# Optimization experiments

Measured on AMD Instinct MI355X. Metric: run time of the kernel, lower is better.

## Reference

```python
import jax, jax.numpy as jnp
import numpy as np

B, S, T, H, VS, VT = 64, 64, 64, 1024, 32000, 32000


def _init(key, shape, scale=0.05):
    return scale * jax.random.normal(key, shape, dtype=jnp.float32)


def setup_inputs() -> dict:
    key = jax.random.key(0)
    ks = jax.random.split(key, 16)
    source = jax.random.randint(ks[0], (B, S), 0, VS)
    target = jax.random.randint(ks[1], (B, T), 0, VT)
    emb_src = _init(ks[2], (VS, H)).at[0].set(0.0)   # padding_idx=0
    emb_tgt = _init(ks[3], (VT, H)).at[0].set(0.0)   # padding_idx=0
    W_ih_enc = _init(ks[4], (4 * H, H)); W_hh_enc = _init(ks[5], (4 * H, H))
    b_ih_enc = _init(ks[6], (4 * H,));   b_hh_enc = _init(ks[7], (4 * H,))
    W_ih_dec = _init(ks[8], (4 * H, H)); W_hh_dec = _init(ks[9], (4 * H, H))
    b_ih_dec = _init(ks[10], (4 * H,));  b_hh_dec = _init(ks[11], (4 * H,))
    W_att = _init(ks[12], (H, 2 * H));   b_att = _init(ks[13], (H,))
    W_out = _init(ks[14], (VT, H));      b_out = _init(ks[15], (VT,))
    return dict(source=source, target=target, emb_src=emb_src, emb_tgt=emb_tgt,
                W_ih_enc=W_ih_enc, W_hh_enc=W_hh_enc, b_ih_enc=b_ih_enc, b_hh_enc=b_hh_enc,
                W_ih_dec=W_ih_dec, W_hh_dec=W_hh_dec, b_ih_dec=b_ih_dec, b_hh_dec=b_hh_dec,
                W_att=W_att, b_att=b_att, W_out=W_out, b_out=b_out)


def _lstm_cell(x, h, c, W_ih, W_hh, b):
    # PyTorch gate order: i, f, g, o
    gates = x @ W_ih.T + h @ W_hh.T + b
    i, f, g, o = jnp.split(gates, 4, axis=-1)
    c_new = jax.nn.sigmoid(f) * c + jax.nn.sigmoid(i) * jnp.tanh(g)
    h_new = jax.nn.sigmoid(o) * jnp.tanh(c_new)
    return h_new, c_new


def reference(source, target, emb_src, emb_tgt,
              W_ih_enc, W_hh_enc, b_ih_enc, b_hh_enc,
              W_ih_dec, W_hh_dec, b_ih_dec, b_hh_dec,
              W_att, b_att, W_out, b_out):
    src = source.T              # [S, B]
    tgt = target.T              # [T, B]
    h0 = jnp.zeros((B, H), jnp.float32)
    c0 = jnp.zeros((B, H), jnp.float32)

    # ---- Encoder: time-major LSTM via scan (dropout in eval mode = identity) ----
    x_src = emb_src[src]        # [S, B, H]
    b_enc = b_ih_enc + b_hh_enc

    def enc_step(carry, x_t):
        h, c = carry
        h, c = _lstm_cell(x_t, h, c, W_ih_enc, W_hh_enc, b_enc)
        return (h, c), h

    (hT, cT), hx_list = jax.lax.scan(enc_step, (h0, c0), x_src)  # hx_list: [S, B, H]

    # ---- Decoder: hx_cx is never updated in the original loop, so every
    # timestep uses the SAME encoder final state -> fully vectorizable over t ----
    words_f = tgt[: S - 1]      # [Td, B], Td = T-1 (S == T)
    words_t = tgt[1:]           # [Td, B]
    x_dec = emb_tgt[words_f]    # [Td, B, H]
    b_dec = b_ih_dec + b_hh_dec
    gates = x_dec @ W_ih_dec.T + (hT @ W_hh_dec.T + b_dec)[None]  # [Td, B, 4H]
    i, f, g, o = jnp.split(gates, 4, axis=-1)
    c_new = jax.nn.sigmoid(f) * cT[None] + jax.nn.sigmoid(i) * jnp.tanh(g)
    hx = jax.nn.sigmoid(o) * jnp.tanh(c_new)                       # [Td, B, H]

    # ---- Attention (dot-product over source positions, softmax over S) ----
    scores = jnp.einsum('tbh,sbh->tsb', hx, hx_list)               # [Td, S, B]
    neg_inf = jnp.asarray(-jnp.inf, jnp.float32)
    mask = (src != 0)[None]                                        # [1, S, B]
    scores = jnp.where(mask, scores, neg_inf)
    align = jax.nn.softmax(scores, axis=1)                         # over S
    content = jnp.einsum('tsb,sbh->tbh', align, hx_list)           # [Td, B, H]
    concat = jnp.concatenate([content, hx], axis=-1)               # [Td, B, 2H]
    hx_att = jnp.tanh(concat @ W_att.T + b_att)                    # [Td, B, H]

    # ---- Output projection + per-step cross entropy (ignore_index=0), summed ----
    logits = hx_att @ W_out.T + b_out                              # [Td, B, VT]
    logp = jax.nn.log_softmax(logits, axis=-1)
    nll = -jnp.take_along_axis(logp, words_t[..., None], axis=-1).squeeze(-1)  # [Td, B]
    valid = (words_t != 0).astype(jnp.float32)
    per_step = jnp.sum(nll * valid, axis=1) / jnp.maximum(jnp.sum(valid, axis=1), 1.0)
    return jnp.sum(per_step)
```

## Files before the change

### kernel.cpp

```cpp
#include <hip/hip_runtime.h>
#include <math.h>

#define Bb 64
#define Ss 64
#define Hh 1024
#define Vv 32000
#define RD 4032
#define RP 4096
#define NT4 4096
#define ENC_NBLK 64

typedef unsigned short u16;
typedef unsigned long long u64;
typedef __attribute__((ext_vector_type(8))) short bf16x8;
typedef __attribute__((ext_vector_type(4))) float f32x4;

#define MFMA(a, b, c) __builtin_amdgcn_mfma_f32_16x16x32_bf16(a, b, c, 0, 0, 0)

__device__ __forceinline__ u16 f2b(float f) {
  union { float f; unsigned u; } v; v.f = f;
  unsigned r = v.u + 0x7fffu + ((v.u >> 16) & 1u);
  return (u16)(r >> 16);
}
__device__ __forceinline__ float b2f(u16 b) {
  union { unsigned u; float f; } v; v.u = ((unsigned)b) << 16; return v.f;
}
__device__ __forceinline__ float sigf(float x) { return 1.f / (1.f + expf(-x)); }

__device__ __forceinline__ u64 AL(const u64* p) {
  return __hip_atomic_load(p, __ATOMIC_RELAXED, __HIP_MEMORY_SCOPE_AGENT);
}
__device__ __forceinline__ void AS(u64* p, u64 v) {
  __hip_atomic_store(p, v, __ATOMIC_RELAXED, __HIP_MEMORY_SCOPE_AGENT);
}
__device__ __forceinline__ int AL32(const int* p) {
  return __hip_atomic_load(p, __ATOMIC_RELAXED, __HIP_MEMORY_SCOPE_AGENT);
}
__device__ __forceinline__ void AS32(int* p, int v) {
  __hip_atomic_store(p, v, __ATOMIC_RELAXED, __HIP_MEMORY_SCOPE_AGENT);
}

__device__ __forceinline__ void gll16(const void* g, void* l) {
  __builtin_amdgcn_global_load_lds(
      (const __attribute__((address_space(1))) unsigned int*)g,
      (__attribute__((address_space(3))) unsigned int*)l, 16, 0, 0);
}

__global__ void k_fail(float* out) { out[0] = 1e30f; }

__global__ void k_cvt(const float* __restrict__ in, u16* __restrict__ out, int n4) {
  int i = blockIdx.x * blockDim.x + threadIdx.x;
  const int st = gridDim.x * blockDim.x;
  for (; i < n4; i += st) {
    float4 v = ((const float4*)in)[i];
    ushort4 o; o.x = f2b(v.x); o.y = f2b(v.y); o.z = f2b(v.z); o.w = f2b(v.w);
    ((ushort4*)out)[i] = o;
  }
}

__global__ void k_gather(const int* __restrict__ tok, const float* __restrict__ emb,
                         u16* __restrict__ outp, int nstep) {
  const int r = blockIdx.x;
  const int step = r >> 6, b = r & 63;
  const int idx = (step < nstep) ? tok[b * 64 + step] : 0;
  const float4 v = ((const float4*)(emb + (size_t)idx * Hh))[threadIdx.x];
  ushort4 o; o.x = f2b(v.x); o.y = f2b(v.y); o.z = f2b(v.z); o.w = f2b(v.w);
  ((ushort4*)(outp + (size_t)r * Hh))[threadIdx.x] = o;
}

__device__ __forceinline__ void dg_tile(const u16* __restrict__ A, const u16* __restrict__ Bm,
                                        u16* __restrict__ C, int bx, int by,
                                        u16* As, u16* Bs) {
  const int tid = threadIdx.x;
  const int wave = tid >> 6, lane = tid & 63;
  const int l15 = lane & 15, lhi = lane >> 4;
  const int m0 = by * 128, n0 = bx * 128;
  const int wm = (wave >> 1) * 64, wn = (wave & 1) * 64;
  f32x4 acc[4][4] = {};
  const int srow = wave * 32 + (lane >> 3);
  const int scolb = (lane & 7) * 16;
  for (int k0 = 0; k0 < Hh; k0 += 64) {
    __syncthreads();
#pragma unroll
    for (int q = 0; q < 4; ++q) {
      const int r = srow + q * 8;
      gll16((const char*)(A + (size_t)(m0 + r) * Hh + k0) + scolb,
            (char*)As + (wave * 32 + q * 8) * 128);
      gll16((const char*)(Bm + (size_t)(n0 + r) * Hh + k0) + scolb,
            (char*)Bs + (wave * 32 + q * 8) * 128);
    }
    __syncthreads();
#pragma unroll
    for (int kk = 0; kk < 2; ++kk) {
      const int ko = kk * 32 + lhi * 8;
      bf16x8 af[4], bfr[4];
#pragma unroll
      for (int i = 0; i < 4; ++i) af[i] = *(const bf16x8*)(As + (wm + i * 16 + l15) * 64 + ko);
#pragma unroll
      for (int j = 0; j < 4; ++j) bfr[j] = *(const bf16x8*)(Bs + (wn + j * 16 + l15) * 64 + ko);
#pragma unroll
      for (int i = 0; i < 4; ++i)
#pragma unroll
        for (int j = 0; j < 4; ++j)
          acc[i][j] = MFMA(af[i], bfr[j], acc[i][j]);
    }
  }
#pragma unroll
  for (int i = 0; i < 4; ++i) {
    const int gr = m0 + wm + i * 16 + lhi * 4;
#pragma unroll
    for (int j = 0; j < 4; ++j) {
      const int gc = n0 + wn + j * 16 + l15;
#pragma unroll
      for (int rr = 0; rr < 4; ++rr)
        C[(size_t)(gr + rr) * NT4 + gc] = f2b(acc[i][j][rr]);
    }
  }
}

__global__ __launch_bounds__(256)
void k_pre(const u16* __restrict__ A, const u16* __restrict__ Bm, u16* __restrict__ C) {
  __shared__ __align__(16) u16 As[128 * 64];
  __shared__ __align__(16) u16 Bs[128 * 64];
  const int t = blockIdx.x;
  dg_tile(A, Bm, C, t & 31, t >> 5, As, Bs);
}

template<int EPI>
__global__ __launch_bounds__(256)
void k_gemm(const u16* __restrict__ A, const u16* __restrict__ Bm,
            void* __restrict__ C, int M, int N, int K,
            const float* __restrict__ bias,
            float* __restrict__ pmax, float* __restrict__ psum, int ncols) {
  __shared__ __align__(16) u16 As[128 * 64];
  __shared__ __align__(16) u16 Bs[128 * 64];
  const int tid = threadIdx.x;
  const int wave = tid >> 6, lane = tid & 63;
  const int l15 = lane & 15, lhi = lane >> 4;
  int bx = blockIdx.x, by = blockIdx.y;
  {
    const int gx_ = gridDim.x, gy_ = gridDim.y;
    const int nwg = gx_ * gy_;
    if ((gy_ & 3) == 0 && (gx_ & 1) == 0) {
      const int f = by * gx_ + bx;
      const int x = f & 7, i = f >> 3;
      const int rby = gy_ >> 2, hx = gx_ >> 1;
      by = (x >> 1) * rby + (i % rby);
      bx = (x & 1) * hx + (i / rby);
    } else if ((nwg & 7) == 0) {
      int flat = by * gx_ + bx;
      const int qq = nwg >> 3;
      flat = (flat & 7) * qq + (flat >> 3);
      bx = flat % gx_; by = flat / gx_;
    }
  }
  const int m0 = by * 128, n0 = bx * 128;
  const int wm = (wave >> 1) * 64, wn = (wave & 1) * 64;
  f32x4 acc[4][4] = {};
  const int srow = wave * 32 + (lane >> 3);
  const int scolb = (lane & 7) * 16;

  for (int k0 = 0; k0 < K; k0 += 64) {
    __syncthreads();
#pragma unroll
    for (int q = 0; q < 4; ++q) {
      const int r = srow + q * 8;
      int ra = m0 + r; ra = (ra < M) ? ra : (M - 1);
      gll16((const char*)(A + (size_t)ra * K + k0) + scolb,
            (char*)As + (wave * 32 + q * 8) * 128);
      gll16((const char*)(Bm + (size_t)(n0 + r) * K + k0) + scolb,
            (char*)Bs + (wave * 32 + q * 8) * 128);
    }
    __syncthreads();
#pragma unroll
    for (int kk = 0; kk < 2; ++kk) {
      const int ko = kk * 32 + lhi * 8;
      bf16x8 af[4], bfr[4];
#pragma unroll
      for (int i = 0; i < 4; ++i) af[i] = *(const bf16x8*)(As + (wm + i * 16 + l15) * 64 + ko);
#pragma unroll
      for (int j = 0; j < 4; ++j) bfr[j] = *(const bf16x8*)(Bs + (wn + j * 16 + l15) * 64 + ko);
#pragma unroll
      for (int i = 0; i < 4; ++i)
#pragma unroll
        for (int j = 0; j < 4; ++j)
          acc[i][j] = MFMA(af[i], bfr[j], acc[i][j]);
    }
  }

  if (EPI == 0) {
#pragma unroll
    for (int i = 0; i < 4; ++i) {
      const int gr = m0 + wm + i * 16 + lhi * 4;
#pragma unroll
      for (int j = 0; j < 4; ++j) {
        const int gc = n0 + wn + j * 16 + l15;
        const float bv = bias ? bias[gc] : 0.f;
#pragma unroll
        for (int rr = 0; rr < 4; ++rr)
          ((float*)C)[(size_t)(gr + rr) * N + gc] = acc[i][j][rr] + bv;
      }
    }
  } else if (EPI == 3) {
#pragma unroll
    for (int i = 0; i < 4; ++i) {
      const int gr = m0 + wm + i * 16 + lhi * 4;
#pragma unroll
      for (int j = 0; j < 4; ++j) {
        const int gc = n0 + wn + j * 16 + l15;
        const float bv = bias[gc];
#pragma unroll
        for (int rr = 0; rr < 4; ++rr)
          ((u16*)C)[(size_t)(gr + rr) * N + gc] = f2b(tanhf(acc[i][j][rr] + bv));
      }
    }
  } else {
    float bj[4];
#pragma unroll
    for (int j = 0; j < 4; ++j) bj[j] = bias[n0 + wn + j * 16 + l15];
    const int pc = bx * 2 + (wn ? 1 : 0);
#pragma unroll
    for (int i = 0; i < 4; ++i) {
#pragma unroll
      for (int rr = 0; rr < 4; ++rr) {
        float v0 = acc[i][0][rr] + bj[0];
        float v1 = acc[i][1][rr] + bj[1];
        float v2 = acc[i][2][rr] + bj[2];
        float v3 = acc[i][3][rr] + bj[3];
        float m = fmaxf(fmaxf(v0, v1), fmaxf(v2, v3));
#pragma unroll
        for (int d = 1; d < 16; d <<= 1) m = fmaxf(m, __shfl_xor(m, d, 64));
        float s = __expf(v0 - m) + __expf(v1 - m) + __expf(v2 - m) + __expf(v3 - m);
#pragma unroll
        for (int d = 1; d < 16; d <<= 1) s += __shfl_xor(s, d, 64);
        if (l15 == 0) {
          const int grow = m0 + wm + i * 16 + lhi * 4 + rr;
          pmax[(size_t)grow * ncols + pc] = m;
          psum[(size_t)grow * ncols + pc] = s;
        }
      }
    }
  }
}

__global__ __launch_bounds__(256, 1)
void k_enc_all(const u16* __restrict__ Wb, const u16* __restrict__ gx,
               const float* __restrict__ b_ih, const float* __restrict__ b_hh,
               u16* __restrict__ hxl, float* __restrict__ c_out, int* flags) {
  __shared__ __align__(16) u16 Ws[64 * 1024];
  __shared__ float Gs[64 * 65];
  __shared__ float bsum[64];
  const int tid = threadIdx.x;
  const int wave = tid >> 6, lane = tid & 63;
  const int l15 = lane & 15, lhi = lane >> 4;
  const int c0 = blockIdx.x * 16;
  const int cb = tid >> 2, cq = tid & 3;
  const int rot = blockIdx.x & 31;

  for (int i = tid; i < 64 * 128; i += 256) {
    const int r = i >> 7, ck = i & 127;
    const int grow = (r >> 4) * Hh + c0 + (r & 15);
    const int bo = (ck * 16) ^ ((r & 7) << 4);
    *(bf16x8*)((char*)Ws + r * 2048 + bo) = *(const bf16x8*)(Wb + (size_t)grow * Hh + ck * 8);
  }
  if (tid < 64) {
    const int col = (tid >> 4) * Hh + c0 + (tid & 15);
    bsum[tid] = b_ih[col] + b_hh[col];
  }
  float creg[4] = {0.f, 0.f, 0.f, 0.f};
  __syncthreads();

  for (int s = 0; s < 64; ++s) {
    u64 graw[4];
#pragma unroll
    for (int g = 0; g < 4; ++g)
      graw[g] = *(const u64*)(gx + (size_t)(s * 64 + cb) * NT4 + g * Hh + c0 + cq * 4);

    f32x4 acc[4] = {};
    if (s > 0) {
      if (wave == 0) {
        for (;;) {
          const int f = AL32(flags + blockIdx.x * 64 + lane);
          if (__all(f >= s)) break;
          __builtin_amdgcn_s_sleep(1);
        }
      }
      __syncthreads();
      const u64* apw = (const u64*)(hxl + ((size_t)(s - 1) * 64 + wave * 16 + l15) * Hh);
      const char* wsb = (const char*)Ws;
      const int xr = (l15 & 7) << 4;
#pragma unroll 8
      for (int i = 0; i < 32; ++i) {
        const int kf = (i + rot) & 31;
        const int k = kf * 32 + lhi * 8;
        const u64 ua = AL(apw + (k >> 2));
        const u64 ub = AL(apw + (k >> 2) + 1);
        union { u64 qq[2]; bf16x8 v; } cv;
        cv.qq[0] = ua; cv.qq[1] = ub;
        const int kb = (k * 2) ^ xr;
#pragma unroll
        for (int nt = 0; nt < 4; ++nt)
          acc[nt] = MFMA(cv.v, *(const bf16x8*)(wsb + (nt * 16 + l15) * 2048 + kb), acc[nt]);
      }
    }
#pragma unroll
    for (int nt = 0; nt < 4; ++nt)
#pragma unroll
      for (int r = 0; r < 4; ++r)
        Gs[(wave * 16 + lhi * 4 + r) * 65 + nt * 16 + l15] = acc[nt][r];
    __syncthreads();
    {
      const float* gsrow = Gs + cb * 65;
      u64 pk = 0;
#pragma unroll
      for (int j = 0; j < 4; ++j) {
        const int col = cq * 4 + j;
        const float gi = gsrow[col]      + b2f((u16)(graw[0] >> (16 * j))) + bsum[col];
        const float gf = gsrow[16 + col] + b2f((u16)(graw[1] >> (16 * j))) + bsum[16 + col];
        const float gg = gsrow[32 + col] + b2f((u16)(graw[2] >> (16 * j))) + bsum[32 + col];
        const float go = gsrow[48 + col] + b2f((u16)(graw[3] >> (16 * j))) + bsum[48 + col];
        const float cn = sigf(gf) * creg[j] + sigf(gi) * tanhf(gg);
        const float hv = sigf(go) * tanhf(cn);
        creg[j] = cn;
        pk |= (u64)f2b(hv) << (16 * j);
      }
      AS((u64*)(hxl + ((size_t)s * 64 + cb) * Hh + c0 + cq * 4), pk);
    }
    __syncthreads();
    if (tid < ENC_NBLK)
      AS32(flags + tid * 64 + blockIdx.x, s + 1);
  }
#pragma unroll
  for (int j = 0; j < 4; ++j)
    c_out[cb * Hh + c0 + cq * 4 + j] = creg[j];
}

__global__ void k_dec_cell(const u16* __restrict__ G, const float* __restrict__ dbase,
                           const float* __restrict__ cT, const float* __restrict__ b_ih,
                           const float* __restrict__ b_hh, u16* __restrict__ Acat) {
  const int idx = blockIdx.x * 256 + threadIdx.x;
  const int r = idx >> 8, c4 = (idx & 255) * 4;
  if (r >= RD) return;
  const int b = r & 63;
  u64 graw[4]; f32x4 dv[4], bi[4], bh[4];
#pragma unroll
  for (int g = 0; g < 4; ++g) {
    graw[g] = *(const u64*)(G + (size_t)r * NT4 + g * Hh + c4);
    dv[g] = *(const f32x4*)(dbase + (size_t)b * NT4 + g * Hh + c4);
    bi[g] = *(const f32x4*)(b_ih + g * Hh + c4);
    bh[g] = *(const f32x4*)(b_hh + g * Hh + c4);
  }
  const f32x4 cv4 = *(const f32x4*)(cT + b * Hh + c4);
  u64 pk = 0;
#pragma unroll
  for (int j = 0; j < 4; ++j) {
    const float gi = b2f((u16)(graw[0] >> (16 * j))) + dv[0][j] + bi[0][j] + bh[0][j];
    const float gf = b2f((u16)(graw[1] >> (16 * j))) + dv[1][j] + bi[1][j] + bh[1][j];
    const float gg = b2f((u16)(graw[2] >> (16 * j))) + dv[2][j] + bi[2][j] + bh[2][j];
    const float go = b2f((u16)(graw[3] >> (16 * j))) + dv[3][j] + bi[3][j] + bh[3][j];
    const float cn = sigf(gf) * cv4[j] + sigf(gi) * tanhf(gg);
    const float hv = sigf(go) * tanhf(cn);
    pk |= (u64)f2b(hv) << (16 * j);
  }
  *(u64*)(Acat + (size_t)r * 2048 + Hh + c4) = pk;
}

__global__ __launch_bounds__(256)
void k_attn(u16* Acat, const u16* __restrict__ hxl, const int* __restrict__ src) {
  __shared__ float qs[Hh];
  __shared__ float sc[Ss];
  const int r = blockIdx.x;
  const int b = r & 63;
  const int tid = threadIdx.x, wave = tid >> 6, lane = tid & 63;
  for (int h = tid; h < Hh; h += 256) qs[h] = b2f(Acat[(size_t)r * 2048 + Hh + h]);
  __syncthreads();
  for (int sub = 0; sub < 16; ++sub) {
    const int ss = wave * 16 + sub;
    const ushort4* hp4 = (const ushort4*)(hxl + ((size_t)ss * Bb + b) * Hh);
    float p = 0.f;
#pragma unroll
    for (int q = 0; q < 4; ++q) {
      const int i4 = lane + 64 * q;
      const ushort4 v = hp4[i4];
      p += qs[i4 * 4 + 0] * b2f(v.x) + qs[i4 * 4 + 1] * b2f(v.y)
         + qs[i4 * 4 + 2] * b2f(v.z) + qs[i4 * 4 + 3] * b2f(v.w);
    }
#pragma unroll
    for (int d = 1; d < 64; d <<= 1) p += __shfl_xor(p, d, 64);
    if (lane == 0) sc[ss] = (src[b * 64 + ss] != 0) ? p : -INFINITY;
  }
  __syncthreads();
  if (wave == 0) {
    const float v = sc[lane];
    float m = v;
#pragma unroll
    for (int d = 1; d < 64; d <<= 1) m = fmaxf(m, __shfl_xor(m, d, 64));
    const float e = __expf(v - m);
    float ssum = e;
#pragma unroll
    for (int d = 1; d < 64; d <<= 1) ssum += __shfl_xor(ssum, d, 64);
    sc[lane] = e / ssum;
  }
  __syncthreads();
  float4 a4 = {0.f, 0.f, 0.f, 0.f};
  for (int s2 = 0; s2 < 64; ++s2) {
    const float a = sc[s2];
    const ushort4 v = *(const ushort4*)(hxl + ((size_t)s2 * Bb + b) * Hh + tid * 4);
    a4.x += a * b2f(v.x); a4.y += a * b2f(v.y);
    a4.z += a * b2f(v.z); a4.w += a * b2f(v.w);
  }
  u16* dst = Acat + (size_t)r * 2048 + tid * 4;
  dst[0] = f2b(a4.x); dst[1] = f2b(a4.y); dst[2] = f2b(a4.z); dst[3] = f2b(a4.w);
}

__global__ void k_lsetl(const float* __restrict__ pmax, const float* __restrict__ psum,
                        const u16* __restrict__ hx_att_b, const int* __restrict__ target,
                        const float* __restrict__ W, const float* __restrict__ bo,
                        float* __restrict__ nll, int ncols) {
  const int r = blockIdx.x * 4 + (threadIdx.x >> 6);
  const int lane = threadIdx.x & 63;
  if (r >= RD) return;
  float m = -INFINITY;
  for (int i = lane; i < ncols; i += 64) m = fmaxf(m, pmax[(size_t)r * ncols + i]);
#pragma unroll
  for (int d = 1; d < 64; d <<= 1) m = fmaxf(m, __shfl_xor(m, d, 64));
  float s = 0.f;
  for (int i = lane; i < ncols; i += 64)
    s += psum[(size_t)r * ncols + i] * __expf(pmax[(size_t)r * ncols + i] - m);
#pragma unroll
  for (int d = 1; d < 64; d <<= 1) s += __shfl_xor(s, d, 64);
  const int t = r >> 6, b = r & 63;
  const int w = target[b * 64 + t + 1];
  const u16* a = hx_att_b + (size_t)r * Hh;
  const float* wr = W + (size_t)w * Hh;
  float p = 0.f;
  for (int h = lane; h < Hh; h += 64) p += b2f(a[h]) * wr[h];
#pragma unroll
  for (int d = 1; d < 64; d <<= 1) p += __shfl_xor(p, d, 64);
  if (lane == 0) nll[r] = (m + logf(s)) - (p + bo[w]);
}

__global__ void k_final(const float* __restrict__ nll, const int* __restrict__ target,
                        float* __restrict__ out) {
  const int t = threadIdx.x;
  float ps = 0.f;
  if (t < 63) {
    float sn = 0.f, cnt = 0.f;
    for (int b = 0; b < 64; ++b) {
      const int r = t * 64 + b;
      const int w = target[b * 64 + t + 1];
      if (w != 0) { sn += nll[r]; cnt += 1.f; }
    }
    ps = sn / fmaxf(cnt, 1.f);
  }
#pragma unroll
  for (int d = 1; d < 64; d <<= 1) ps += __shfl_xor(ps, d, 64);
  if (t == 0) out[0] = ps;
}

extern "C" void kernel_launch(void* const* d_in, const int* in_sizes, int n_in,
                              void* d_out, int out_size, void* d_ws, size_t ws_size,
                              hipStream_t stream) {
  const int*   source   = (const int*)d_in[0];
  const int*   target   = (const int*)d_in[1];
  const float* emb_src  = (const float*)d_in[2];
  const float* emb_tgt  = (const float*)d_in[3];
  const float* W_ih_enc = (const float*)d_in[4];
  const float* W_hh_enc = (const float*)d_in[5];
  const float* b_ih_enc = (const float*)d_in[6];
  const float* b_hh_enc = (const float*)d_in[7];
  const float* W_ih_dec = (const float*)d_in[8];
  const float* W_hh_dec = (const float*)d_in[9];
  const float* b_ih_dec = (const float*)d_in[10];
  const float* b_hh_dec = (const float*)d_in[11];
  const float* W_att    = (const float*)d_in[12];
  const float* b_att    = (const float*)d_in[13];
  const float* W_out    = (const float*)d_in[14];
  const float* b_out    = (const float*)d_in[15];
  float* out = (float*)d_out;

  char* base = (char*)d_ws;
  size_t off = 0;
  auto alloc = [&](size_t bytes) -> void* {
    void* r = base + off; off += (bytes + 255) & ~(size_t)255; return r;
  };
  u16*   wb_ih_enc = (u16*)alloc((size_t)NT4 * Hh * 2);
  u16*   wb_hh_enc = (u16*)alloc((size_t)NT4 * Hh * 2);
  u16*   wb_ih_dec = (u16*)alloc((size_t)NT4 * Hh * 2);
  u16*   wb_hh_dec = (u16*)alloc((size_t)NT4 * Hh * 2);
  u16*   wb_att    = (u16*)alloc((size_t)Hh * 2048 * 2);
  u16*   wb_out    = (u16*)alloc((size_t)Vv * Hh * 2);
  u16*   x_src_b   = (u16*)alloc((size_t)RP * Hh * 2);
  u16*   x_dec_b   = (u16*)alloc((size_t)RP * Hh * 2);
  u16*   gates16   = (u16*)alloc((size_t)RP * NT4 * 2);
  u16*   gates_dec = (u16*)alloc((size_t)RP * NT4 * 2);
  u16*   hxl       = (u16*)alloc((size_t)Ss * Bb * Hh * 2);
  float* c_enc     = (float*)alloc((size_t)Bb * Hh * 4);
  float* dbase     = (float*)alloc((size_t)128 * NT4 * 4);
  u16*   Acat      = (u16*)alloc((size_t)RP * 2048 * 2);
  u16*   hx_att_b  = (u16*)alloc((size_t)RP * Hh * 2);
  float* pmax      = (float*)alloc((size_t)RP * 500 * 4);
  float* psum      = (float*)alloc((size_t)RP * 500 * 4);
  float* nll       = (float*)alloc((size_t)RD * 4);
  int*   flags     = (int*)alloc(ENC_NBLK * ENC_NBLK * 4);

  if (off > ws_size) { k_fail<<<1, 1, 0, stream>>>(out); return; }

  k_cvt<<<2048, 256, 0, stream>>>(W_ih_enc, wb_ih_enc, NT4 * Hh / 4);
  k_cvt<<<2048, 256, 0, stream>>>(W_hh_enc, wb_hh_enc, NT4 * Hh / 4);
  k_cvt<<<2048, 256, 0, stream>>>(W_ih_dec, wb_ih_dec, NT4 * Hh / 4);
  k_cvt<<<2048, 256, 0, stream>>>(W_hh_dec, wb_hh_dec, NT4 * Hh / 4);
  k_cvt<<<2048, 256, 0, stream>>>(W_att, wb_att, Hh * 2048 / 4);
  k_cvt<<<2048, 256, 0, stream>>>(W_out, wb_out, Vv * Hh / 4);

  hipMemsetAsync(flags, 0, ENC_NBLK * ENC_NBLK * 4, stream);

  k_gather<<<RP, 256, 0, stream>>>(source, emb_src, x_src_b, 64);
  k_gather<<<RP, 256, 0, stream>>>(target, emb_tgt, x_dec_b, 63);

  k_pre<<<1024, 256, 0, stream>>>(x_src_b, wb_ih_enc, gates16);
  k_enc_all<<<ENC_NBLK, 256, 0, stream>>>(wb_hh_enc, gates16, b_ih_enc, b_hh_enc,
                                          hxl, c_enc, flags);

  k_pre<<<1024, 256, 0, stream>>>(x_dec_b, wb_ih_dec, gates_dec);
  k_gemm<0><<<dim3(32, 1), 256, 0, stream>>>(hxl + (size_t)63 * Bb * Hh, wb_hh_dec, dbase,
                                             64, NT4, Hh, nullptr, nullptr, nullptr, 0);
  k_dec_cell<<<RD, 256, 0, stream>>>(gates_dec, dbase, c_enc, b_ih_dec, b_hh_dec, Acat);

  k_attn<<<RD, 256, 0, stream>>>(Acat, hxl, source);

  k_gemm<3><<<dim3(8, 32), 256, 0, stream>>>(Acat, wb_att, hx_att_b, RP, Hh, 2048,
                                             b_att, nullptr, nullptr, 0);

  k_gemm<2><<<dim3(250, 32), 256, 0, stream>>>(hx_att_b, wb_out, nullptr, RP, Vv, Hh,
                                               b_out, pmax, psum, 500);
  k_lsetl<<<(RD + 3) / 4, 256, 0, stream>>>(pmax, psum, hx_att_b, target, W_out, b_out,
                                            nll, 500);
  k_final<<<1, 64, 0, stream>>>(nll, target, out);
}
```

Before: 1.522 ms.

## Merge prep launches and stage encoder states in LDS for attention

```diff
diff --git a/kernel.cpp b/kernel.cpp
--- a/kernel.cpp
+++ b/kernel.cpp
@@ -48,19 +48,39 @@
 
 __global__ void k_fail(float* out) { out[0] = 1e30f; }
 
-__global__ void k_cvt(const float* __restrict__ in, u16* __restrict__ out, int n4) {
-  int i = blockIdx.x * blockDim.x + threadIdx.x;
+__global__ void k_cvt_all(const float* __restrict__ s0, u16* __restrict__ d0,
+                          const float* __restrict__ s1, u16* __restrict__ d1,
+                          const float* __restrict__ s2, u16* __restrict__ d2,
+                          const float* __restrict__ s3, u16* __restrict__ d3,
+                          const float* __restrict__ s4, u16* __restrict__ d4,
+                          const float* __restrict__ s5, u16* __restrict__ d5) {
+  const int A4 = NT4 * Hh / 4;
+  const int E4 = Hh * 2048 / 4;
+  const int F4 = Vv * Hh / 4;
+  const int TOT = 4 * A4 + E4 + F4;
   const int st = gridDim.x * blockDim.x;
-  for (; i < n4; i += st) {
-    float4 v = ((const float4*)in)[i];
+  for (int i = blockIdx.x * blockDim.x + threadIdx.x; i < TOT; i += st) {
+    const float* sp; u16* dp; int off;
+    if (i < A4)            { sp = s0; dp = d0; off = i; }
+    else if (i < 2 * A4)   { sp = s1; dp = d1; off = i - A4; }
+    else if (i < 3 * A4)   { sp = s2; dp = d2; off = i - 2 * A4; }
+    else if (i < 4 * A4)   { sp = s3; dp = d3; off = i - 3 * A4; }
+    else if (i < 4 * A4 + E4) { sp = s4; dp = d4; off = i - 4 * A4; }
+    else                   { sp = s5; dp = d5; off = i - 4 * A4 - E4; }
+    const float4 v = ((const float4*)sp)[off];
     ushort4 o; o.x = f2b(v.x); o.y = f2b(v.y); o.z = f2b(v.z); o.w = f2b(v.w);
-    ((ushort4*)out)[i] = o;
-  }
-}
-
-__global__ void k_gather(const int* __restrict__ tok, const float* __restrict__ emb,
-                         u16* __restrict__ outp, int nstep) {
-  const int r = blockIdx.x;
+    ((ushort4*)dp)[off] = o;
+  }
+}
+
+__global__ void k_gather2(const int* __restrict__ src_tok, const float* __restrict__ emb_s,
+                          u16* __restrict__ out_s,
+                          const int* __restrict__ tgt_tok, const float* __restrict__ emb_t,
+                          u16* __restrict__ out_t) {
+  int r = blockIdx.x;
+  const int* tok; const float* emb; u16* outp; int nstep;
+  if (r < RP) { tok = src_tok; emb = emb_s; outp = out_s; nstep = 64; }
+  else        { r -= RP; tok = tgt_tok; emb = emb_t; outp = out_t; nstep = 63; }
   const int step = r >> 6, b = r & 63;
   const int idx = (step < nstep) ? tok[b * 64 + step] : 0;
   const float4 v = ((const float4*)(emb + (size_t)idx * Hh))[threadIdx.x];
@@ -119,11 +139,13 @@
 }
 
 __global__ __launch_bounds__(256)
-void k_pre(const u16* __restrict__ A, const u16* __restrict__ Bm, u16* __restrict__ C) {
+void k_pre2(const u16* __restrict__ Ae, const u16* __restrict__ Be, u16* __restrict__ Ce,
+            const u16* __restrict__ Ad, const u16* __restrict__ Bd, u16* __restrict__ Cd) {
   __shared__ __align__(16) u16 As[128 * 64];
   __shared__ __align__(16) u16 Bs[128 * 64];
-  const int t = blockIdx.x;
-  dg_tile(A, Bm, C, t & 31, t >> 5, As, Bs);
+  int t = blockIdx.x;
+  if (t < 1024) dg_tile(Ae, Be, Ce, t & 31, t >> 5, As, Bs);
+  else { t -= 1024; dg_tile(Ad, Bd, Cd, t & 31, t >> 5, As, Bs); }
 }
 
 template<int EPI>
@@ -366,51 +388,73 @@
 }
 
 __global__ __launch_bounds__(256)
-void k_attn(u16* Acat, const u16* __restrict__ hxl, const int* __restrict__ src) {
-  __shared__ float qs[Hh];
-  __shared__ float sc[Ss];
-  const int r = blockIdx.x;
-  const int b = r & 63;
+void k_attn_b(u16* __restrict__ Acat, const u16* __restrict__ hxl,
+              const int* __restrict__ src) {
+  __shared__ __align__(16) u16 hs[64 * 1024];
+  __shared__ float qs[1024];
+  __shared__ float prob[64];
+  __shared__ int mflag[64];
+  const int b = blockIdx.x >> 2, th = blockIdx.x & 3;
   const int tid = threadIdx.x, wave = tid >> 6, lane = tid & 63;
-  for (int h = tid; h < Hh; h += 256) qs[h] = b2f(Acat[(size_t)r * 2048 + Hh + h]);
+#pragma unroll 8
+  for (int i = 0; i < 32; ++i) {
+    const int c = i * 4 + wave;
+    gll16((const char*)(hxl + ((size_t)(c >> 1) * 64 + b) * Hh + (c & 1) * 512) + lane * 16,
+          (char*)hs + c * 1024 + lane * 16);
+  }
+  if (tid < 64) mflag[tid] = (src[b * 64 + tid] != 0);
   __syncthreads();
-  for (int sub = 0; sub < 16; ++sub) {
-    const int ss = wave * 16 + sub;
-    const ushort4* hp4 = (const ushort4*)(hxl + ((size_t)ss * Bb + b) * Hh);
-    float p = 0.f;
-#pragma unroll
-    for (int q = 0; q < 4; ++q) {
-      const int i4 = lane + 64 * q;
-      const ushort4 v = hp4[i4];
-      p += qs[i4 * 4 + 0] * b2f(v.x) + qs[i4 * 4 + 1] * b2f(v.y)
-         + qs[i4 * 4 + 2] * b2f(v.z) + qs[i4 * 4 + 3] * b2f(v.w);
-    }
-#pragma unroll
-    for (int d = 1; d < 64; d <<= 1) p += __shfl_xor(p, d, 64);
-    if (lane == 0) sc[ss] = (src[b * 64 + ss] != 0) ? p : -INFINITY;
-  }
-  __syncthreads();
-  if (wave == 0) {
-    const float v = sc[lane];
-    float m = v;
-#pragma unroll
-    for (int d = 1; d < 64; d <<= 1) m = fmaxf(m, __shfl_xor(m, d, 64));
-    const float e = __expf(v - m);
-    float ssum = e;
-#pragma unroll
-    for (int d = 1; d < 64; d <<= 1) ssum += __shfl_xor(ssum, d, 64);
-    sc[lane] = e / ssum;
-  }
-  __syncthreads();
-  float4 a4 = {0.f, 0.f, 0.f, 0.f};
-  for (int s2 = 0; s2 < 64; ++s2) {
-    const float a = sc[s2];
-    const ushort4 v = *(const ushort4*)(hxl + ((size_t)s2 * Bb + b) * Hh + tid * 4);
-    a4.x += a * b2f(v.x); a4.y += a * b2f(v.y);
-    a4.z += a * b2f(v.z); a4.w += a * b2f(v.w);
-  }
-  u16* dst = Acat + (size_t)r * 2048 + tid * 4;
-  dst[0] = f2b(a4.x); dst[1] = f2b(a4.y); dst[2] = f2b(a4.z); dst[3] = f2b(a4.w);
+  const int t0 = th * 16;
+  const int tEnd = (t0 + 16 < 63) ? t0 + 16 : 63;
+  for (int t = t0; t < tEnd; ++t) {
+    const size_t r = (size_t)t * 64 + b;
+    {
+      const u64 q4 = *(const u64*)(Acat + r * 2048 + Hh + tid * 4);
+      qs[tid * 4 + 0] = b2f((u16)q4);
+      qs[tid * 4 + 1] = b2f((u16)(q4 >> 16));
+      qs[tid * 4 + 2] = b2f((u16)(q4 >> 32));
+      qs[tid * 4 + 3] = b2f((u16)(q4 >> 48));
+    }
+    __syncthreads();
+    for (int sub = 0; sub < 16; ++sub) {
+      const int ss = wave * 16 + sub;
+      float p = 0.f;
+#pragma unroll
+      for (int q = 0; q < 4; ++q) {
+        const int i4 = lane + 64 * q;
+        const ushort4 v = *(const ushort4*)(hs + ss * 1024 + i4 * 4);
+        p += qs[i4 * 4 + 0] * b2f(v.x) + qs[i4 * 4 + 1] * b2f(v.y)
+           + qs[i4 * 4 + 2] * b2f(v.z) + qs[i4 * 4 + 3] * b2f(v.w);
+      }
+#pragma unroll
+      for (int d = 1; d < 64; d <<= 1) p += __shfl_xor(p, d, 64);
+      if (lane == 0) prob[ss] = mflag[ss] ? p : -INFINITY;
+    }
+    __syncthreads();
+    if (wave == 0) {
+      const float v = prob[lane];
+      float m = v;
+#pragma unroll
+      for (int d = 1; d < 64; d <<= 1) m = fmaxf(m, __shfl_xor(m, d, 64));
+      const float e = __expf(v - m);
+      float ssum = e;
+#pragma unroll
+      for (int d = 1; d < 64; d <<= 1) ssum += __shfl_xor(ssum, d, 64);
+      prob[lane] = e / ssum;
+    }
+    __syncthreads();
+    float4 a4 = {0.f, 0.f, 0.f, 0.f};
+    for (int s2 = 0; s2 < 64; ++s2) {
+      const float a = prob[s2];
+      const ushort4 v = *(const ushort4*)(hs + s2 * 1024 + tid * 4);
+      a4.x += a * b2f(v.x); a4.y += a * b2f(v.y);
+      a4.z += a * b2f(v.z); a4.w += a * b2f(v.w);
+    }
+    const u64 pk = (u64)f2b(a4.x) | ((u64)f2b(a4.y) << 16)
+                 | ((u64)f2b(a4.z) << 32) | ((u64)f2b(a4.w) << 48);
+    *(u64*)(Acat + r * 2048 + tid * 4) = pk;
+    __syncthreads();
+  }
 }
 
 __global__ void k_lsetl(const float* __restrict__ pmax, const float* __restrict__ psum,
@@ -506,28 +550,26 @@
 
   if (off > ws_size) { k_fail<<<1, 1, 0, stream>>>(out); return; }
 
-  k_cvt<<<2048, 256, 0, stream>>>(W_ih_enc, wb_ih_enc, NT4 * Hh / 4);
-  k_cvt<<<2048, 256, 0, stream>>>(W_hh_enc, wb_hh_enc, NT4 * Hh / 4);
-  k_cvt<<<2048, 256, 0, stream>>>(W_ih_dec, wb_ih_dec, NT4 * Hh / 4);
-  k_cvt<<<2048, 256, 0, stream>>>(W_hh_dec, wb_hh_dec, NT4 * Hh / 4);
-  k_cvt<<<2048, 256, 0, stream>>>(W_att, wb_att, Hh * 2048 / 4);
-  k_cvt<<<2048, 256, 0, stream>>>(W_out, wb_out, Vv * Hh / 4);
+  k_cvt_all<<<2048, 256, 0, stream>>>(W_ih_enc, wb_ih_enc, W_hh_enc, wb_hh_enc,
+                                      W_ih_dec, wb_ih_dec, W_hh_dec, wb_hh_dec,
+                                      W_att, wb_att, W_out, wb_out);
 
   hipMemsetAsync(flags, 0, ENC_NBLK * ENC_NBLK * 4, stream);
 
-  k_gather<<<RP, 256, 0, stream>>>(source, emb_src, x_src_b, 64);
-  k_gather<<<RP, 256, 0, stream>>>(target, emb_tgt, x_dec_b, 63);
-
-  k_pre<<<1024, 256, 0, stream>>>(x_src_b, wb_ih_enc, gates16);
+  k_gather2<<<2 * RP, 256, 0, stream>>>(source, emb_src, x_src_b,
+                                        target, emb_tgt, x_dec_b);
+
+  k_pre2<<<2048, 256, 0, stream>>>(x_src_b, wb_ih_enc, gates16,
+                                   x_dec_b, wb_ih_dec, gates_dec);
+
   k_enc_all<<<ENC_NBLK, 256, 0, stream>>>(wb_hh_enc, gates16, b_ih_enc, b_hh_enc,
                                           hxl, c_enc, flags);
 
-  k_pre<<<1024, 256, 0, stream>>>(x_dec_b, wb_ih_dec, gates_dec);
   k_gemm<0><<<dim3(32, 1), 256, 0, stream>>>(hxl + (size_t)63 * Bb * Hh, wb_hh_dec, dbase,
                                              64, NT4, Hh, nullptr, nullptr, nullptr, 0);
   k_dec_cell<<<RD, 256, 0, stream>>>(gates_dec, dbase, c_enc, b_ih_dec, b_hh_dec, Acat);
 
-  k_attn<<<RD, 256, 0, stream>>>(Acat, hxl, source);
+  k_attn_b<<<256, 256, 0, stream>>>(Acat, hxl, source);
 
   k_gemm<3><<<dim3(8, 32), 256, 0, stream>>>(Acat, wb_att, hx_att_b, RP, Hh, 2048,
                                              b_att, nullptr, nullptr, 0);
```

Measured after the change: 1.571 ms. 1.03x slower.
